# Kernel optimization log

Hardware: AMD Instinct MI355X
Metric: run time of the kernel (lower is better)

Reference implementation:

```python
import jax, jax.numpy as jnp
import numpy as np

D_MODEL = 1024
N_HEADS = 16
D_K = D_MODEL // N_HEADS
B, T = 2, 2048


def setup_inputs() -> dict:
    key = jax.random.key(0)
    ks = jax.random.split(key, 12)
    s = 0.02
    return {
        "q": jax.random.normal(ks[0], (B, T, D_MODEL), jnp.float32),
        "k": jax.random.normal(ks[1], (B, T, D_MODEL), jnp.float32),
        "v": jax.random.normal(ks[2], (B, T, D_MODEL), jnp.float32),
        "Wq": jax.random.normal(ks[3], (D_MODEL, D_MODEL), jnp.float32) * s,
        "bq": jnp.zeros((D_MODEL,), jnp.float32),
        "Wk": jax.random.normal(ks[4], (D_MODEL, D_MODEL), jnp.float32) * s,
        "bk": jnp.zeros((D_MODEL,), jnp.float32),
        "Wv": jax.random.normal(ks[5], (D_MODEL, D_MODEL), jnp.float32) * s,
        "bv": jnp.zeros((D_MODEL,), jnp.float32),
        "Wo": jax.random.normal(ks[6], (D_MODEL, D_MODEL), jnp.float32) * s,
        "bo": jnp.zeros((D_MODEL,), jnp.float32),
        "mask": jnp.ones((B, T), jnp.int32),
        "causal": 1,
    }


def reference(q, k, v, Wq, bq, Wk, bk, Wv, bv, Wo, bo, mask, causal):
    Bq, Tq, D = q.shape
    Tk = k.shape[1]
    # projections (torch Linear: x @ W.T + b), split heads -> [B, H, T, d_k]
    qh = (q @ Wq.T + bq).reshape(Bq, Tq, N_HEADS, D_K).transpose(0, 2, 1, 3)
    kh = (k @ Wk.T + bk).reshape(Bq, Tk, N_HEADS, D_K).transpose(0, 2, 1, 3)
    vh = (v @ Wv.T + bv).reshape(Bq, Tk, N_HEADS, D_K).transpose(0, 2, 1, 3)
    scores = jnp.einsum("bhqd,bhkd->bhqk", qh, kh) / jnp.sqrt(jnp.float32(D_K))
    neg_inf = jnp.float32(-jnp.inf)
    if mask is not None:
        scores = jnp.where(mask[:, None, None, :] == 0, neg_inf, scores)
    if causal:
        causal_mask = jnp.tril(jnp.ones((Tq, Tq), jnp.float32))
        scores = jnp.where(causal_mask == 0, neg_inf, scores)
    attn = jax.nn.softmax(scores, axis=-1)
    out = jnp.einsum("bhqk,bhkd->bhqd", attn, vh)
    out = out.transpose(0, 2, 1, 3).reshape(Bq, Tq, D)
    return out @ Wo.T + bo
```

## Files before the change

kernel.cpp:

```cpp
#include <hip/hip_runtime.h>
#include <cstdint>
#include <cstddef>


typedef __bf16 bf16x8 __attribute__((ext_vector_type(8)));
typedef float f32x4 __attribute__((ext_vector_type(4)));

#define MFMA(a, b, c) __builtin_amdgcn_mfma_f32_16x16x32_bf16((a), (b), (c), 0, 0, 0)

static constexpr int D_MODEL = 1024;
static constexpr int T_ = 2048;
static constexpr int M_TOK = 4096;

__device__ __forceinline__ unsigned short f32_to_bf16(float f) {
    union { float f; uint32_t u; } v; v.f = f;
    uint32_t u = v.u;
    uint32_t r = u + 0x7fffu + ((u >> 16) & 1u);
    return (unsigned short)(r >> 16);
}

typedef __attribute__((address_space(1))) void* as1_ptr;
typedef __attribute__((address_space(3))) void* as3_ptr;
__device__ __forceinline__ void gload_lds16(const void* g, void* l) {
    __builtin_amdgcn_global_load_lds((as1_ptr)(void*)g, (as3_ptr)l, 16, 0, 0);
}

__global__ void cvt_all(const float* __restrict__ q, const float* __restrict__ k,
                        const float* __restrict__ v, const float* __restrict__ wq,
                        const float* __restrict__ wk, const float* __restrict__ wv,
                        const float* __restrict__ wo, ushort4* __restrict__ dst) {
    int i = blockIdx.x * blockDim.x + threadIdx.x;
    constexpr int R = 1 << 20;
    if (i >= 4 * R) return;
    const float* srcs[7] = {q, k, v, wq, wk, wv, wo};
    int region, idx;
    if (i < 3 * R) { region = i >> 20; idx = i & (R - 1); }
    else { int j = i - 3 * R; region = 3 + (j >> 18); idx = j & ((1 << 18) - 1); }
    float4 f = ((const float4*)srcs[region])[idx];
    ushort4 o;
    o.x = f32_to_bf16(f.x); o.y = f32_to_bf16(f.y);
    o.z = f32_to_bf16(f.z); o.w = f32_to_bf16(f.w);
    dst[i] = o;
}

template<int MODE>
__device__ __forceinline__ void gemm_body(
    const unsigned short* __restrict__ A, const unsigned short* __restrict__ W,
    const float* __restrict__ bias, void* __restrict__ outp,
    unsigned short* As, unsigned short* Ws, int bx, int by)
{
    const int tid = threadIdx.x;
    const int lane = tid & 63, wave = tid >> 6;
    const int wm = wave >> 1, wn = wave & 1;
    const int r16 = lane & 15, kg = lane >> 4;
    const int m_blk = by * 128, n_blk = bx * 64;

    f32x4 acc[4][2];
    #pragma unroll
    for (int mt = 0; mt < 4; ++mt)
        #pragma unroll
        for (int nt = 0; nt < 2; ++nt) acc[mt][nt] = (f32x4){0, 0, 0, 0};

    for (int k0 = 0; k0 < D_MODEL; k0 += 64) {
        __syncthreads();
        #pragma unroll
        for (int j = 0; j < 4; ++j) {
            int si = j * 256 + tid;
            int row = si >> 3, cg = (si & 7) ^ (row & 7);
            gload_lds16(A + (size_t)(m_blk + row) * D_MODEL + k0 + cg * 8,
                        (char*)As + (j * 256 + wave * 64) * 16);
        }
        #pragma unroll
        for (int j = 0; j < 2; ++j) {
            int si = j * 256 + tid;
            int row = si >> 3, cg = (si & 7) ^ (row & 7);
            gload_lds16(W + (size_t)(n_blk + row) * D_MODEL + k0 + cg * 8,
                        (char*)Ws + (j * 256 + wave * 64) * 16);
        }
        __syncthreads();
        #pragma unroll
        for (int kc = 0; kc < 2; ++kc) {
            bf16x8 af[4], wf[2];
            #pragma unroll
            for (int mt = 0; mt < 4; ++mt) {
                int row = wm * 64 + mt * 16 + r16;
                af[mt] = *(const bf16x8*)(As + row * 64 + (((kc * 4 + kg) ^ (row & 7)) * 8));
            }
            #pragma unroll
            for (int nt = 0; nt < 2; ++nt) {
                int row = wn * 32 + nt * 16 + r16;
                wf[nt] = *(const bf16x8*)(Ws + row * 64 + (((kc * 4 + kg) ^ (row & 7)) * 8));
            }
            #pragma unroll
            for (int mt = 0; mt < 4; ++mt)
                #pragma unroll
                for (int nt = 0; nt < 2; ++nt)
                    acc[mt][nt] = MFMA(af[mt], wf[nt], acc[mt][nt]);
        }
    }
    #pragma unroll
    for (int nt = 0; nt < 2; ++nt) {
        int n = n_blk + wn * 32 + nt * 16 + r16;
        float bn = bias[n];
        #pragma unroll
        for (int mt = 0; mt < 4; ++mt)
            #pragma unroll
            for (int r = 0; r < 4; ++r) {
                int m = m_blk + wm * 64 + mt * 16 + kg * 4 + r;
                float vv = acc[mt][nt][r] + bn;
                if (MODE == 3) {
                    ((float*)outp)[(size_t)m * D_MODEL + n] = vv;
                } else {
                    int b = m >> 11, t = m & 2047, h = n >> 6, dki = n & 63;
                    unsigned short* o = (unsigned short*)outp;
                    if (MODE == 0)
                        o[((size_t)(b * 16 + h) * 2048 + t) * 64 + dki] = f32_to_bf16(vv);
                    else
                        o[((size_t)(b * 16 + h) * 64 + dki) * 2048 + t] = f32_to_bf16(vv);
                }
            }
    }
}

__global__ __launch_bounds__(256) void gemm_qkv(
    const unsigned short* __restrict__ qb, const unsigned short* __restrict__ kb,
    const unsigned short* __restrict__ vb, const unsigned short* __restrict__ Wqb,
    const unsigned short* __restrict__ Wkb, const unsigned short* __restrict__ Wvb,
    const float* __restrict__ bq, const float* __restrict__ bk, const float* __restrict__ bv,
    unsigned short* __restrict__ Qhp, unsigned short* __restrict__ Khp,
    unsigned short* __restrict__ Vtp)
{
    __shared__ __align__(16) unsigned short As[128 * 64];
    __shared__ __align__(16) unsigned short Ws[64 * 64];
    const int z = blockIdx.z;
    const unsigned short* A = (z == 0) ? qb : (z == 1) ? kb : vb;
    const unsigned short* W = (z == 0) ? Wqb : (z == 1) ? Wkb : Wvb;
    const float* bias = (z == 0) ? bq : (z == 1) ? bk : bv;
    if (z < 2)
        gemm_body<0>(A, W, bias, (z == 0) ? (void*)Qhp : (void*)Khp, As, Ws,
                     blockIdx.x, blockIdx.y);
    else
        gemm_body<2>(A, W, bias, (void*)Vtp, As, Ws, blockIdx.x, blockIdx.y);
}

__global__ __launch_bounds__(256) void gemm_out(
    const unsigned short* __restrict__ ab, const unsigned short* __restrict__ Wob,
    const float* __restrict__ bo, float* __restrict__ outp)
{
    __shared__ __align__(16) unsigned short As[128 * 64];
    __shared__ __align__(16) unsigned short Ws[64 * 64];
    gemm_body<3>(ab, Wob, bo, (void*)outp, As, Ws, blockIdx.x, blockIdx.y);
}

__global__ __launch_bounds__(256) void attn_fwd(
    const unsigned short* __restrict__ Qh, const unsigned short* __restrict__ Kh,
    const unsigned short* __restrict__ Vt, const int* __restrict__ mask,
    const int* __restrict__ causal_p, unsigned short* __restrict__ attnout)
{
    __shared__ __align__(16) unsigned short Ks[64 * 64];
    __shared__ __align__(16) unsigned short Vs[64 * 64];
    __shared__ __align__(16) unsigned short Ps[4][16 * 64];

    const int tid = threadIdx.x;
    const int lane = tid & 63, wave = tid >> 6;
    const int qc = blockIdx.x, bh = blockIdx.y;
    const int b = bh >> 4, h = bh & 15;
    const int q0 = qc * 64 + wave * 16;
    const int causal = *causal_p;
    const int r16 = lane & 15, kg = lane >> 4;

    const unsigned short* Qb = Qh + (size_t)bh * T_ * 64;
    const unsigned short* Kb = Kh + (size_t)bh * T_ * 64;
    const unsigned short* Vb = Vt + (size_t)bh * 64 * T_;
    const int* mb = mask + b * T_;

    bf16x8 qf0 = *(const bf16x8*)(Qb + (size_t)(q0 + r16) * 64 + kg * 8);
    bf16x8 qf1 = *(const bf16x8*)(Qb + (size_t)(q0 + r16) * 64 + 32 + kg * 8);

    float lacc[4] = {0.f, 0.f, 0.f, 0.f};
    f32x4 o[4];
    #pragma unroll
    for (int f = 0; f < 4; ++f) o[f] = (f32x4){0, 0, 0, 0};
    const float sc2 = 0.18033688011112042f;

    const int kend = causal ? (qc * 64 + 64) : T_;
    for (int t0 = 0; t0 < kend; t0 += 64) {
        __syncthreads();
        #pragma unroll
        for (int j = 0; j < 2; ++j) {
            int si = j * 256 + tid;
            int row = si >> 3, cg = (si & 7) ^ (row & 7);
            gload_lds16(Kb + (size_t)(t0 + row) * 64 + cg * 8,
                        (char*)Ks + (j * 256 + wave * 64) * 16);
            gload_lds16(Vb + (size_t)row * T_ + t0 + cg * 8,
                        (char*)Vs + (j * 256 + wave * 64) * 16);
        }
        __syncthreads();

        f32x4 s[4];
        #pragma unroll
        for (int c = 0; c < 4; ++c) {
            int key = c * 16 + r16;
            bf16x8 kf0 = *(const bf16x8*)(Ks + key * 64 + ((kg ^ (key & 7)) * 8));
            bf16x8 kf1 = *(const bf16x8*)(Ks + key * 64 + (((4 + kg) ^ (key & 7)) * 8));
            f32x4 z = (f32x4){0, 0, 0, 0};
            z = MFMA(qf0, kf0, z);
            z = MFMA(qf1, kf1, z);
            s[c] = z;
        }

        const bool needc = causal && (t0 + 64 > q0);
        float p[4][4];
        #pragma unroll
        for (int c = 0; c < 4; ++c) {
            int kcol = t0 + c * 16 + r16;
            bool mok = (mb[kcol] != 0);
            #pragma unroll
            for (int r = 0; r < 4; ++r) {
                int qrow = q0 + kg * 4 + r;
                bool ok = mok && (!needc || (kcol <= qrow));
                p[c][r] = ok ? __builtin_amdgcn_exp2f(s[c][r] * sc2) : 0.f;
            }
        }
        #pragma unroll
        for (int r = 0; r < 4; ++r)
            lacc[r] += (p[0][r] + p[1][r]) + (p[2][r] + p[3][r]);

        unsigned short* pw = Ps[wave];
        #pragma unroll
        for (int c = 0; c < 4; ++c)
            #pragma unroll
            for (int r = 0; r < 4; ++r) {
                int row = kg * 4 + r, col = c * 16 + r16;
                pw[row * 64 + (((col >> 3) ^ (row & 7)) * 8 + (col & 7))] =
                    f32_to_bf16(p[c][r]);
            }
        __asm__ volatile("s_waitcnt lgkmcnt(0)" ::: "memory");
        bf16x8 pf0 = *(const bf16x8*)(pw + r16 * 64 + ((kg ^ (r16 & 7)) * 8));
        bf16x8 pf1 = *(const bf16x8*)(pw + r16 * 64 + (((4 + kg) ^ (r16 & 7)) * 8));

        #pragma unroll
        for (int f = 0; f < 4; ++f) {
            int n = f * 16 + r16;
            bf16x8 vf0 = *(const bf16x8*)(Vs + n * 64 + ((kg ^ (n & 7)) * 8));
            bf16x8 vf1 = *(const bf16x8*)(Vs + n * 64 + (((4 + kg) ^ (n & 7)) * 8));
            o[f] = MFMA(pf0, vf0, o[f]);
            o[f] = MFMA(pf1, vf1, o[f]);
        }
    }

    #pragma unroll
    for (int r = 0; r < 4; ++r) {
        float lv = lacc[r];
        #pragma unroll
        for (int off = 1; off < 16; off <<= 1) lv += __shfl_xor(lv, off, 64);
        float inv = (lv > 0.f) ? 1.0f / lv : 0.f;
        int qrow = q0 + kg * 4 + r;
        size_t base = ((size_t)(b * T_ + qrow)) * D_MODEL + h * 64;
        #pragma unroll
        for (int f = 0; f < 4; ++f)
            attnout[base + f * 16 + r16] = f32_to_bf16(o[f][r] * inv);
    }
}

extern "C" void kernel_launch(void* const* d_in, const int* in_sizes, int n_in,
                              void* d_out, int out_size, void* d_ws, size_t ws_size,
                              hipStream_t stream) {
    const float* q  = (const float*)d_in[0];
    const float* k  = (const float*)d_in[1];
    const float* v  = (const float*)d_in[2];
    const float* Wq = (const float*)d_in[3];
    const float* bq = (const float*)d_in[4];
    const float* Wk = (const float*)d_in[5];
    const float* bk = (const float*)d_in[6];
    const float* Wv = (const float*)d_in[7];
    const float* bv = (const float*)d_in[8];
    const float* Wo = (const float*)d_in[9];
    const float* bo = (const float*)d_in[10];
    const int* mask   = (const int*)d_in[11];
    const int* causal = (const int*)d_in[12];

    const size_t SZ_TOK = (size_t)M_TOK * D_MODEL;
    const size_t SZ_W   = (size_t)D_MODEL * D_MODEL;

    unsigned short* qb  = (unsigned short*)d_ws;
    unsigned short* kb  = qb  + SZ_TOK;
    unsigned short* vb  = kb  + SZ_TOK;
    unsigned short* Wqb = vb  + SZ_TOK;
    unsigned short* Wkb = Wqb + SZ_W;
    unsigned short* Wvb = Wkb + SZ_W;
    unsigned short* Wob = Wvb + SZ_W;
    unsigned short* Qhp = Wob + SZ_W;
    unsigned short* Khp = Qhp + SZ_TOK;
    unsigned short* Vtp = Khp + SZ_TOK;
    unsigned short* ab  = Vtp + SZ_TOK;

    cvt_all<<<16384, 256, 0, stream>>>(q, k, v, Wq, Wk, Wv, Wo, (ushort4*)qb);

    gemm_qkv<<<dim3(D_MODEL / 64, M_TOK / 128, 3), 256, 0, stream>>>(
        qb, kb, vb, Wqb, Wkb, Wvb, bq, bk, bv, Qhp, Khp, Vtp);

    attn_fwd<<<dim3(32, 32), 256, 0, stream>>>(Qhp, Khp, Vtp, mask, causal, ab);

    gemm_out<<<dim3(D_MODEL / 64, M_TOK / 128), 256, 0, stream>>>(ab, Wob, bo,
                                                                  (float*)d_out);
}
```

Measured before the change: 260.7 us.

## Pair causal query blocks, double-buffer K/V, and widen GEMM tiles to 128x128

The attention kernel now has each block process two query chunks (p and 31-p) so causal work is balanced across blocks and each K/V tile is reused by both. K/V tiles are double-buffered so the next tile's global-to-LDS load overlaps the current compute. The GEMMs move from 128x64 to 128x128 tiles for more operand reuse per block, and the convert kernel drops its indexed pointer array. The P conversion uses a cheaper, slightly less exact bf16 rounding. These changes raise register and LDS use and halve the attention grid, which may lower occupancy.

```diff
diff --git a/kernel.cpp b/kernel.cpp
--- a/kernel.cpp
+++ b/kernel.cpp
@@ -18,6 +18,10 @@
     uint32_t r = u + 0x7fffu + ((u >> 16) & 1u);
     return (unsigned short)(r >> 16);
 }
+__device__ __forceinline__ unsigned short f32_to_bf16_fast(float f) {
+    union { float f; uint32_t u; } v; v.f = f;
+    return (unsigned short)((v.u + 0x8000u) >> 16);
+}
 
 typedef __attribute__((address_space(1))) void* as1_ptr;
 typedef __attribute__((address_space(3))) void* as3_ptr;
@@ -25,18 +29,25 @@
     __builtin_amdgcn_global_load_lds((as1_ptr)(void*)g, (as3_ptr)l, 16, 0, 0);
 }
 
-__global__ void cvt_all(const float* __restrict__ q, const float* __restrict__ k,
-                        const float* __restrict__ v, const float* __restrict__ wq,
-                        const float* __restrict__ wk, const float* __restrict__ wv,
-                        const float* __restrict__ wo, ushort4* __restrict__ dst) {
+__global__ __launch_bounds__(256) void cvt_all(
+    const float* __restrict__ q, const float* __restrict__ k,
+    const float* __restrict__ v, const float* __restrict__ wq,
+    const float* __restrict__ wk, const float* __restrict__ wv,
+    const float* __restrict__ wo, ushort4* __restrict__ dst) {
     int i = blockIdx.x * blockDim.x + threadIdx.x;
     constexpr int R = 1 << 20;
-    if (i >= 4 * R) return;
-    const float* srcs[7] = {q, k, v, wq, wk, wv, wo};
-    int region, idx;
-    if (i < 3 * R) { region = i >> 20; idx = i & (R - 1); }
-    else { int j = i - 3 * R; region = 3 + (j >> 18); idx = j & ((1 << 18) - 1); }
-    float4 f = ((const float4*)srcs[region])[idx];
+    const float* s;
+    int idx;
+    if (i < 3 * R) {
+        s = (i < R) ? q : (i < 2 * R) ? k : v;
+        idx = i & (R - 1);
+    } else {
+        int j = i - 3 * R;
+        int w = j >> 18;
+        s = (w == 0) ? wq : (w == 1) ? wk : (w == 2) ? wv : wo;
+        idx = j & ((1 << 18) - 1);
+    }
+    float4 f = ((const float4*)s)[idx];
     ushort4 o;
     o.x = f32_to_bf16(f.x); o.y = f32_to_bf16(f.y);
     o.z = f32_to_bf16(f.z); o.w = f32_to_bf16(f.w);
@@ -53,13 +64,13 @@
     const int lane = tid & 63, wave = tid >> 6;
     const int wm = wave >> 1, wn = wave & 1;
     const int r16 = lane & 15, kg = lane >> 4;
-    const int m_blk = by * 128, n_blk = bx * 64;
-
-    f32x4 acc[4][2];
+    const int m_blk = by * 128, n_blk = bx * 128;
+
+    f32x4 acc[4][4];
     #pragma unroll
     for (int mt = 0; mt < 4; ++mt)
         #pragma unroll
-        for (int nt = 0; nt < 2; ++nt) acc[mt][nt] = (f32x4){0, 0, 0, 0};
+        for (int nt = 0; nt < 4; ++nt) acc[mt][nt] = (f32x4){0, 0, 0, 0};
 
     for (int k0 = 0; k0 < D_MODEL; k0 += 64) {
         __syncthreads();
@@ -71,7 +82,7 @@
                         (char*)As + (j * 256 + wave * 64) * 16);
         }
         #pragma unroll
-        for (int j = 0; j < 2; ++j) {
+        for (int j = 0; j < 4; ++j) {
             int si = j * 256 + tid;
             int row = si >> 3, cg = (si & 7) ^ (row & 7);
             gload_lds16(W + (size_t)(n_blk + row) * D_MODEL + k0 + cg * 8,
@@ -80,27 +91,27 @@
         __syncthreads();
         #pragma unroll
         for (int kc = 0; kc < 2; ++kc) {
-            bf16x8 af[4], wf[2];
+            bf16x8 af[4], wf[4];
             #pragma unroll
             for (int mt = 0; mt < 4; ++mt) {
                 int row = wm * 64 + mt * 16 + r16;
                 af[mt] = *(const bf16x8*)(As + row * 64 + (((kc * 4 + kg) ^ (row & 7)) * 8));
             }
             #pragma unroll
-            for (int nt = 0; nt < 2; ++nt) {
-                int row = wn * 32 + nt * 16 + r16;
+            for (int nt = 0; nt < 4; ++nt) {
+                int row = wn * 64 + nt * 16 + r16;
                 wf[nt] = *(const bf16x8*)(Ws + row * 64 + (((kc * 4 + kg) ^ (row & 7)) * 8));
             }
             #pragma unroll
             for (int mt = 0; mt < 4; ++mt)
                 #pragma unroll
-                for (int nt = 0; nt < 2; ++nt)
+                for (int nt = 0; nt < 4; ++nt)
                     acc[mt][nt] = MFMA(af[mt], wf[nt], acc[mt][nt]);
         }
     }
     #pragma unroll
-    for (int nt = 0; nt < 2; ++nt) {
-        int n = n_blk + wn * 32 + nt * 16 + r16;
+    for (int nt = 0; nt < 4; ++nt) {
+        int n = n_blk + wn * 64 + nt * 16 + r16;
         float bn = bias[n];
         #pragma unroll
         for (int mt = 0; mt < 4; ++mt)
@@ -131,7 +142,7 @@
     unsigned short* __restrict__ Vtp)
 {
     __shared__ __align__(16) unsigned short As[128 * 64];
-    __shared__ __align__(16) unsigned short Ws[64 * 64];
+    __shared__ __align__(16) unsigned short Ws[128 * 64];
     const int z = blockIdx.z;
     const unsigned short* A = (z == 0) ? qb : (z == 1) ? kb : vb;
     const unsigned short* W = (z == 0) ? Wqb : (z == 1) ? Wkb : Wvb;
@@ -148,7 +159,7 @@
     const float* __restrict__ bo, float* __restrict__ outp)
 {
     __shared__ __align__(16) unsigned short As[128 * 64];
-    __shared__ __align__(16) unsigned short Ws[64 * 64];
+    __shared__ __align__(16) unsigned short Ws[128 * 64];
     gemm_body<3>(ab, Wob, bo, (void*)outp, As, Ws, blockIdx.x, blockIdx.y);
 }
 
@@ -157,109 +168,157 @@
     const unsigned short* __restrict__ Vt, const int* __restrict__ mask,
     const int* __restrict__ causal_p, unsigned short* __restrict__ attnout)
 {
-    __shared__ __align__(16) unsigned short Ks[64 * 64];
-    __shared__ __align__(16) unsigned short Vs[64 * 64];
-    __shared__ __align__(16) unsigned short Ps[4][16 * 64];
+    __shared__ __align__(16) unsigned short Ks[2][64 * 64];
+    __shared__ __align__(16) unsigned short Vs[2][64 * 64];
+    __shared__ __align__(16) unsigned short PsA[4][16 * 64];
+    __shared__ __align__(16) unsigned short PsB[4][16 * 64];
 
     const int tid = threadIdx.x;
     const int lane = tid & 63, wave = tid >> 6;
-    const int qc = blockIdx.x, bh = blockIdx.y;
+    const int p = blockIdx.x, bh = blockIdx.y;
     const int b = bh >> 4, h = bh & 15;
-    const int q0 = qc * 64 + wave * 16;
     const int causal = *causal_p;
     const int r16 = lane & 15, kg = lane >> 4;
+
+    const int qcA = p, qcB = 31 - p;
+    const int q0A = qcA * 64 + wave * 16;
+    const int q0B = qcB * 64 + wave * 16;
 
     const unsigned short* Qb = Qh + (size_t)bh * T_ * 64;
     const unsigned short* Kb = Kh + (size_t)bh * T_ * 64;
     const unsigned short* Vb = Vt + (size_t)bh * 64 * T_;
     const int* mb = mask + b * T_;
 
-    bf16x8 qf0 = *(const bf16x8*)(Qb + (size_t)(q0 + r16) * 64 + kg * 8);
-    bf16x8 qf1 = *(const bf16x8*)(Qb + (size_t)(q0 + r16) * 64 + 32 + kg * 8);
-
-    float lacc[4] = {0.f, 0.f, 0.f, 0.f};
-    f32x4 o[4];
+    bf16x8 qfA0 = *(const bf16x8*)(Qb + (size_t)(q0A + r16) * 64 + kg * 8);
+    bf16x8 qfA1 = *(const bf16x8*)(Qb + (size_t)(q0A + r16) * 64 + 32 + kg * 8);
+    bf16x8 qfB0 = *(const bf16x8*)(Qb + (size_t)(q0B + r16) * 64 + kg * 8);
+    bf16x8 qfB1 = *(const bf16x8*)(Qb + (size_t)(q0B + r16) * 64 + 32 + kg * 8);
+
+    float laccA[4] = {0, 0, 0, 0}, laccB[4] = {0, 0, 0, 0};
+    f32x4 oA[4], oB[4];
     #pragma unroll
-    for (int f = 0; f < 4; ++f) o[f] = (f32x4){0, 0, 0, 0};
+    for (int f = 0; f < 4; ++f) { oA[f] = (f32x4){0,0,0,0}; oB[f] = (f32x4){0,0,0,0}; }
     const float sc2 = 0.18033688011112042f;
 
-    const int kend = causal ? (qc * 64 + 64) : T_;
-    for (int t0 = 0; t0 < kend; t0 += 64) {
-        __syncthreads();
+    const int nT = causal ? (qcB + 1) : 32;
+
+    auto stage = [&](int buf, int t) {
+        int t0 = t * 64;
         #pragma unroll
         for (int j = 0; j < 2; ++j) {
             int si = j * 256 + tid;
             int row = si >> 3, cg = (si & 7) ^ (row & 7);
             gload_lds16(Kb + (size_t)(t0 + row) * 64 + cg * 8,
-                        (char*)Ks + (j * 256 + wave * 64) * 16);
+                        (char*)Ks[buf] + (j * 256 + wave * 64) * 16);
             gload_lds16(Vb + (size_t)row * T_ + t0 + cg * 8,
-                        (char*)Vs + (j * 256 + wave * 64) * 16);
-        }
+                        (char*)Vs[buf] + (j * 256 + wave * 64) * 16);
+        }
+    };
+
+    stage(0, 0);
+    for (int t = 0; t < nT; ++t) {
         __syncthreads();
-
-        f32x4 s[4];
+        if (t + 1 < nT) stage((t + 1) & 1, t + 1);
+        const unsigned short* Kst = Ks[t & 1];
+        const unsigned short* Vst = Vs[t & 1];
+        const int t0 = t * 64;
+        const bool activeA = !causal || (t <= qcA);
+        const bool needcA = causal && (t == qcA);
+        const bool needcB = causal && (t == qcB);
+
+        f32x4 sA[4], sB[4];
         #pragma unroll
         for (int c = 0; c < 4; ++c) {
             int key = c * 16 + r16;
-            bf16x8 kf0 = *(const bf16x8*)(Ks + key * 64 + ((kg ^ (key & 7)) * 8));
-            bf16x8 kf1 = *(const bf16x8*)(Ks + key * 64 + (((4 + kg) ^ (key & 7)) * 8));
-            f32x4 z = (f32x4){0, 0, 0, 0};
-            z = MFMA(qf0, kf0, z);
-            z = MFMA(qf1, kf1, z);
-            s[c] = z;
-        }
-
-        const bool needc = causal && (t0 + 64 > q0);
-        float p[4][4];
+            bf16x8 kf0 = *(const bf16x8*)(Kst + key * 64 + ((kg ^ (key & 7)) * 8));
+            bf16x8 kf1 = *(const bf16x8*)(Kst + key * 64 + (((4 + kg) ^ (key & 7)) * 8));
+            f32x4 zB = (f32x4){0,0,0,0};
+            zB = MFMA(qfB0, kf0, zB);
+            zB = MFMA(qfB1, kf1, zB);
+            sB[c] = zB;
+            if (activeA) {
+                f32x4 zA = (f32x4){0,0,0,0};
+                zA = MFMA(qfA0, kf0, zA);
+                zA = MFMA(qfA1, kf1, zA);
+                sA[c] = zA;
+            }
+        }
+
+        float pA[4][4], pB[4][4];
         #pragma unroll
         for (int c = 0; c < 4; ++c) {
             int kcol = t0 + c * 16 + r16;
-            bool mok = (mb[kcol] != 0);
+            bool mk = (mb[kcol] != 0);
             #pragma unroll
             for (int r = 0; r < 4; ++r) {
-                int qrow = q0 + kg * 4 + r;
-                bool ok = mok && (!needc || (kcol <= qrow));
-                p[c][r] = ok ? __builtin_amdgcn_exp2f(s[c][r] * sc2) : 0.f;
-            }
-        }
-        #pragma unroll
-        for (int r = 0; r < 4; ++r)
-            lacc[r] += (p[0][r] + p[1][r]) + (p[2][r] + p[3][r]);
-
-        unsigned short* pw = Ps[wave];
+                bool okB = mk && (!needcB || (kcol <= q0B + kg * 4 + r));
+                pB[c][r] = okB ? __builtin_amdgcn_exp2f(sB[c][r] * sc2) : 0.f;
+            }
+            if (activeA) {
+                #pragma unroll
+                for (int r = 0; r < 4; ++r) {
+                    bool okA = mk && (!needcA || (kcol <= q0A + kg * 4 + r));
+                    pA[c][r] = okA ? __builtin_amdgcn_exp2f(sA[c][r] * sc2) : 0.f;
+                }
+            }
+        }
+        #pragma unroll
+        for (int r = 0; r < 4; ++r) {
+            laccB[r] += (pB[0][r] + pB[1][r]) + (pB[2][r] + pB[3][r]);
+            if (activeA) laccA[r] += (pA[0][r] + pA[1][r]) + (pA[2][r] + pA[3][r]);
+        }
+
+        unsigned short* pwA = PsA[wave];
+        unsigned short* pwB = PsB[wave];
         #pragma unroll
         for (int c = 0; c < 4; ++c)
             #pragma unroll
             for (int r = 0; r < 4; ++r) {
                 int row = kg * 4 + r, col = c * 16 + r16;
-                pw[row * 64 + (((col >> 3) ^ (row & 7)) * 8 + (col & 7))] =
-                    f32_to_bf16(p[c][r]);
+                int addr = row * 64 + (((col >> 3) ^ (row & 7)) * 8 + (col & 7));
+                pwB[addr] = f32_to_bf16_fast(pB[c][r]);
+                if (activeA) pwA[addr] = f32_to_bf16_fast(pA[c][r]);
             }
         __asm__ volatile("s_waitcnt lgkmcnt(0)" ::: "memory");
-        bf16x8 pf0 = *(const bf16x8*)(pw + r16 * 64 + ((kg ^ (r16 & 7)) * 8));
-        bf16x8 pf1 = *(const bf16x8*)(pw + r16 * 64 + (((4 + kg) ^ (r16 & 7)) * 8));
+        bf16x8 pfB0 = *(const bf16x8*)(pwB + r16 * 64 + ((kg ^ (r16 & 7)) * 8));
+        bf16x8 pfB1 = *(const bf16x8*)(pwB + r16 * 64 + (((4 + kg) ^ (r16 & 7)) * 8));
+        bf16x8 pfA0, pfA1;
+        if (activeA) {
+            pfA0 = *(const bf16x8*)(pwA + r16 * 64 + ((kg ^ (r16 & 7)) * 8));
+            pfA1 = *(const bf16x8*)(pwA + r16 * 64 + (((4 + kg) ^ (r16 & 7)) * 8));
+        }
 
         #pragma unroll
         for (int f = 0; f < 4; ++f) {
             int n = f * 16 + r16;
-            bf16x8 vf0 = *(const bf16x8*)(Vs + n * 64 + ((kg ^ (n & 7)) * 8));
-            bf16x8 vf1 = *(const bf16x8*)(Vs + n * 64 + (((4 + kg) ^ (n & 7)) * 8));
-            o[f] = MFMA(pf0, vf0, o[f]);
-            o[f] = MFMA(pf1, vf1, o[f]);
+            bf16x8 vf0 = *(const bf16x8*)(Vst + n * 64 + ((kg ^ (n & 7)) * 8));
+            bf16x8 vf1 = *(const bf16x8*)(Vst + n * 64 + (((4 + kg) ^ (n & 7)) * 8));
+            oB[f] = MFMA(pfB0, vf0, oB[f]);
+            oB[f] = MFMA(pfB1, vf1, oB[f]);
+            if (activeA) {
+                oA[f] = MFMA(pfA0, vf0, oA[f]);
+                oA[f] = MFMA(pfA1, vf1, oA[f]);
+            }
         }
     }
 
     #pragma unroll
     for (int r = 0; r < 4; ++r) {
-        float lv = lacc[r];
-        #pragma unroll
-        for (int off = 1; off < 16; off <<= 1) lv += __shfl_xor(lv, off, 64);
-        float inv = (lv > 0.f) ? 1.0f / lv : 0.f;
-        int qrow = q0 + kg * 4 + r;
-        size_t base = ((size_t)(b * T_ + qrow)) * D_MODEL + h * 64;
-        #pragma unroll
-        for (int f = 0; f < 4; ++f)
-            attnout[base + f * 16 + r16] = f32_to_bf16(o[f][r] * inv);
+        float lA = laccA[r], lB = laccB[r];
+        #pragma unroll
+        for (int off = 1; off < 16; off <<= 1) {
+            lA += __shfl_xor(lA, off, 64);
+            lB += __shfl_xor(lB, off, 64);
+        }
+        float invA = (lA > 0.f) ? 1.0f / lA : 0.f;
+        float invB = (lB > 0.f) ? 1.0f / lB : 0.f;
+        size_t baseA = ((size_t)(b * T_ + q0A + kg * 4 + r)) * D_MODEL + h * 64;
+        size_t baseB = ((size_t)(b * T_ + q0B + kg * 4 + r)) * D_MODEL + h * 64;
+        #pragma unroll
+        for (int f = 0; f < 4; ++f) {
+            attnout[baseA + f * 16 + r16] = f32_to_bf16(oA[f][r] * invA);
+            attnout[baseB + f * 16 + r16] = f32_to_bf16(oB[f][r] * invB);
+        }
     }
 }
 
@@ -297,11 +356,11 @@
 
     cvt_all<<<16384, 256, 0, stream>>>(q, k, v, Wq, Wk, Wv, Wo, (ushort4*)qb);
 
-    gemm_qkv<<<dim3(D_MODEL / 64, M_TOK / 128, 3), 256, 0, stream>>>(
+    gemm_qkv<<<dim3(D_MODEL / 128, M_TOK / 128, 3), 256, 0, stream>>>(
         qb, kb, vb, Wqb, Wkb, Wvb, bq, bk, bv, Qhp, Khp, Vtp);
 
-    attn_fwd<<<dim3(32, 32), 256, 0, stream>>>(Qhp, Khp, Vtp, mask, causal, ab);
-
-    gemm_out<<<dim3(D_MODEL / 64, M_TOK / 128), 256, 0, stream>>>(ab, Wob, bo,
-                                                                  (float*)d_out);
-}
+    attn_fwd<<<dim3(16, 32), 256, 0, stream>>>(Qhp, Khp, Vtp, mask, causal, ab);
+
+    gemm_out<<<dim3(D_MODEL / 128, M_TOK / 128), 256, 0, stream>>>(ab, Wob, bo,
+                                                                   (float*)d_out);
+}
```

Measured after the change: 278.8 us. 1.07x slower.
